# Performance work log

Hardware: AMD Instinct MI355X
Metric: run time of the kernel (lower is better)

Reference implementation:

```python
import jax, jax.numpy as jnp
import numpy as np


@jax.custom_vjp
def binarize_ste(x):
    return jnp.sign(x)


def _binarize_fwd(x):
    return jnp.sign(x), None


def _binarize_bwd(_, g):
    # straight-through estimator: pass gradient through, clamped to [-1, 1]
    return (jnp.clip(g, -1.0, 1.0),)


binarize_ste.defvjp(_binarize_fwd, _binarize_bwd)


def setup_inputs() -> dict:
    key = jax.random.key(0)
    kx, kw = jax.random.split(key)
    x = jax.random.normal(kx, (32, 128, 64, 64), dtype=jnp.float32)  # NCHW
    weight = jax.random.normal(kw, (256, 128, 3, 3), dtype=jnp.float32)  # OIHW
    return {"x": x, "weight": weight}


def reference(x, weight):
    w_bin = binarize_ste(weight)  # +/-1 (0 where weight==0, matching torch.sign)
    out = jax.lax.conv_general_dilated(
        x, w_bin,
        window_strides=(1, 1),
        padding=((1, 1), (1, 1)),
        dimension_numbers=("NCHW", "OIHW", "NCHW"),
    )
    return out
```

## Files before the change

### kernel.cpp

```cpp
#include <hip/hip_runtime.h>
#include <hip/hip_bf16.h>


typedef short bf16x8 __attribute__((ext_vector_type(8)));
typedef float f32x4 __attribute__((ext_vector_type(4)));

#define XT_ELEMS (32 * 66 * 66 * 128)
#define XT_BYTES (XT_ELEMS * 2)

__device__ __forceinline__ void glds16(const void* g, const void* l) {
    __builtin_amdgcn_global_load_lds(
        (const __attribute__((address_space(1))) void*)g,
        (__attribute__((address_space(3))) void*)l, 16, 0, 0);
}

__global__ void prep_w_kernel(const float* __restrict__ w,
                              __hip_bfloat16* __restrict__ wm) {
    int tid = blockIdx.x * 256 + threadIdx.x;
    int o = tid / 1152;
    int r = tid - o * 1152;
    int j = r >> 7;
    int c = r & 127;
    float v = w[o * 1152 + c * 9 + j];
    float s = (v > 0.f) ? 1.f : ((v < 0.f) ? -1.f : 0.f);
    wm[tid] = __float2bfloat16(s);
}

__global__ void transpose_x_kernel(const float* __restrict__ x,
                                   __hip_bfloat16* __restrict__ xt) {
    __shared__ short tl[64 * 130];
    const int t = threadIdx.x;
    const int n = blockIdx.x >> 6;
    const int h = blockIdx.x & 63;
    const float* xp = x + (size_t)n * 524288 + h * 64;
    for (int i = t; i < 8192; i += 256) {
        int w = i & 63, c = i >> 6;
        tl[w * 130 + c] = (short)__bfloat16_as_ushort(__float2bfloat16(xp[c * 4096 + w]));
    }
    uint* xtn = (uint*)(xt + (size_t)n * 66 * 66 * 128);
    {
        int row = h + 1;
        if (t < 64)       xtn[(row * 66 + 0) * 64 + t] = 0u;
        else if (t < 128) xtn[(row * 66 + 65) * 64 + (t - 64)] = 0u;
    }
    if (h == 0)  for (int i = t; i < 66 * 64; i += 256) xtn[i] = 0u;
    if (h == 63) for (int i = t; i < 66 * 64; i += 256) xtn[65 * 66 * 64 + i] = 0u;
    __syncthreads();
    uint* xo = (uint*)(xt + ((size_t)(n * 66 + h + 1) * 66 + 1) * 128);
    for (int i = t; i < 4096; i += 256) {
        int c2 = i & 63;
        int w = i >> 6;
        xo[w * 64 + c2] = *(const uint*)(tl + w * 130 + c2 * 2);
    }
}

__global__ __launch_bounds__(256, 2) void gemm_kernel(
    const __hip_bfloat16* __restrict__ xt,
    const __hip_bfloat16* __restrict__ wm,
    float* __restrict__ out) {
    __shared__ short As[128 * 64];
    __shared__ short Bw[2112 * 8];

    const int t = threadIdx.x;
    const int lane = t & 63;
    const int wv = t >> 6;
    const int px_blk = blockIdx.x;
    const int o_blk = blockIdx.y;
    const int n = px_blk >> 4;
    const int h0 = (px_blk & 15) * 4;

    const int wo = (wv & 1) * 64;
    const int wp = (wv >> 1) * 128;
    const int wpr = wp >> 6;
    const int l15 = lane & 15;
    const int quad = lane >> 4;
    const int srow = lane >> 3;
    const int sseg = lane & 7;

    const short* wmS = (const short*)wm + (o_blk * 128) * 1152;
    const short* xtS = (const short*)xt;

    f32x4 acc[4][8] = {};

    for (int cc = 0; cc < 128; cc += 64) {
        for (int kh = 0; kh < 3; ++kh) {
            const short* xw = xtS + ((size_t)(n * 66 + h0 + kh) * 66) * 128;
#pragma unroll
            for (int i = 0; i < 9; ++i) {
                int bidx = i * 4 + wv;
                if (bidx < 33) {
                    int l = bidx * 64 + lane;
                    int cell = l >> 3;
                    int q = l & 7;
                    int s = q ^ (cell & 7);
                    glds16(xw + cell * 128 + cc + s * 8, Bw + bidx * 512);
                }
            }
            for (int kw = 0; kw < 3; ++kw) {
                const int j = kh * 3 + kw;
#pragma unroll
                for (int i = 0; i < 4; ++i) {
                    int r0 = wv * 32 + i * 8;
                    int r = r0 + srow;
                    int segl = sseg ^ (r & 7);
                    glds16(wmS + r * 1152 + j * 128 + cc + segl * 8,
                           As + r0 * 64);
                }
                __syncthreads();
#pragma unroll
                for (int kf = 0; kf < 2; ++kf) {
                    bf16x8 a[4], b[8];
#pragma unroll
                    for (int i = 0; i < 4; ++i) {
                        int o = wo + i * 16 + l15;
                        int seg = (kf * 4 + quad) ^ (o & 7);
                        a[i] = *(const bf16x8*)(As + o * 64 + seg * 8);
                    }
#pragma unroll
                    for (int i = 0; i < 8; ++i) {
                        int cell = (wpr + (i >> 2)) * 66 + (i & 3) * 16 + l15 + kw;
                        int seg = (kf * 4 + quad) ^ (cell & 7);
                        b[i] = *(const bf16x8*)(Bw + cell * 64 + seg * 8);
                    }
#pragma unroll
                    for (int i = 0; i < 4; ++i)
#pragma unroll
                        for (int jj = 0; jj < 8; ++jj)
                            acc[i][jj] = __builtin_amdgcn_mfma_f32_16x16x32_bf16(
                                a[i], b[jj], acc[i][jj], 0, 0, 0);
                }
                __syncthreads();
            }
        }
    }

    const int Pbase = px_blk * 256 + wp;
#pragma unroll
    for (int i = 0; i < 4; ++i) {
#pragma unroll
        for (int jj = 0; jj < 8; ++jj) {
            const int P = Pbase + jj * 16 + l15;
            const int hw = P & 4095;
            float* op = out + (size_t)n * 1048576 + hw;
#pragma unroll
            for (int r = 0; r < 4; ++r) {
                const int o = o_blk * 128 + wo + i * 16 + quad * 4 + r;
                op[(size_t)o * 4096] = acc[i][jj][r];
            }
        }
    }
}

extern "C" void kernel_launch(void* const* d_in, const int* in_sizes, int n_in,
                              void* d_out, int out_size, void* d_ws, size_t ws_size,
                              hipStream_t stream) {
    const float* x = (const float*)d_in[0];
    const float* w = (const float*)d_in[1];
    float* out = (float*)d_out;
    __hip_bfloat16* xt = (__hip_bfloat16*)d_ws;
    __hip_bfloat16* wm = (__hip_bfloat16*)((char*)d_ws + XT_BYTES);

    prep_w_kernel<<<1152, 256, 0, stream>>>(w, wm);
    transpose_x_kernel<<<2048, 256, 0, stream>>>(x, xt);
    gemm_kernel<<<dim3(512, 2), 256, 0, stream>>>(xt, wm, out);
}
```

Measured before the change: 249.0 us.

## Double-buffer LDS staging, widen blocks to all 256 outputs, swizzle block order

The GEMM kernel now uses 512-thread blocks that cover all 256 output channels, so each input tile is loaded once instead of once per output-channel half. Weight and input tiles are double-buffered in LDS with 32-channel K-steps, and the next stage is prefetched while MFMAs run on the current one. This leaves one barrier per step where there were two. Block indices are permuted to spread neighbouring pixel tiles across the grid. The cost is larger LDS use (about 100KB per block), which may limit occupancy to one block per CU despite the launch bounds of 2.

```diff
diff --git a/kernel.cpp b/kernel.cpp
--- a/kernel.cpp
+++ b/kernel.cpp
@@ -54,87 +54,102 @@
     }
 }
 
-__global__ __launch_bounds__(256, 2) void gemm_kernel(
+__global__ __launch_bounds__(512, 2) void gemm_kernel(
     const __hip_bfloat16* __restrict__ xt,
     const __hip_bfloat16* __restrict__ wm,
     float* __restrict__ out) {
-    __shared__ short As[128 * 64];
-    __shared__ short Bw[2112 * 8];
+    __shared__ short As[2][256 * 32];
+    __shared__ short Bw[2][264 * 64];
 
     const int t = threadIdx.x;
     const int lane = t & 63;
     const int wv = t >> 6;
-    const int px_blk = blockIdx.x;
-    const int o_blk = blockIdx.y;
-    const int n = px_blk >> 4;
-    const int h0 = (px_blk & 15) * 4;
-
-    const int wo = (wv & 1) * 64;
-    const int wp = (wv >> 1) * 128;
-    const int wpr = wp >> 6;
     const int l15 = lane & 15;
     const int quad = lane >> 4;
-    const int srow = lane >> 3;
-    const int sseg = lane & 7;
 
-    const short* wmS = (const short*)wm + (o_blk * 128) * 1152;
-    const short* xtS = (const short*)xt;
+    const int bid = blockIdx.x;
+    const int px_blk = (bid & 7) * 64 + (bid >> 3);
+    const int n = px_blk >> 4;
+    const int h0 = (px_blk & 15) << 2;
+
+    const int wo = (wv >> 1) * 64;
+    const int wpr = (wv & 1) * 2;
+
+    const short* wmS = (const short*)wm;
+    const short* xtS = (const short*)xt + (size_t)(n * 66 + h0) * 66 * 128;
 
     f32x4 acc[4][8] = {};
 
-    for (int cc = 0; cc < 128; cc += 64) {
-        for (int kh = 0; kh < 3; ++kh) {
-            const short* xw = xtS + ((size_t)(n * 66 + h0 + kh) * 66) * 128;
+    auto stageA = [&](int buf, int cc, int j) {
+        const short* src = wmS + j * 128 + cc;
 #pragma unroll
-            for (int i = 0; i < 9; ++i) {
-                int bidx = i * 4 + wv;
-                if (bidx < 33) {
-                    int l = bidx * 64 + lane;
-                    int cell = l >> 3;
-                    int q = l & 7;
-                    int s = q ^ (cell & 7);
-                    glds16(xw + cell * 128 + cc + s * 8, Bw + bidx * 512);
-                }
-            }
-            for (int kw = 0; kw < 3; ++kw) {
-                const int j = kh * 3 + kw;
+        for (int i = 0; i < 2; ++i) {
+            int g = i * 8 + wv;
+            int l = g * 64 + lane;
+            int o = l >> 2, q = l & 3;
+            glds16(src + o * 1152 + ((q ^ (o & 3)) * 8), &As[buf][g * 512]);
+        }
+    };
+    auto stageB = [&](int buf, int cc, int kh) {
+        const short* src = xtS + kh * (66 * 128) + cc;
 #pragma unroll
-                for (int i = 0; i < 4; ++i) {
-                    int r0 = wv * 32 + i * 8;
-                    int r = r0 + srow;
-                    int segl = sseg ^ (r & 7);
-                    glds16(wmS + r * 1152 + j * 128 + cc + segl * 8,
-                           As + r0 * 64);
-                }
-                __syncthreads();
-#pragma unroll
-                for (int kf = 0; kf < 2; ++kf) {
-                    bf16x8 a[4], b[8];
-#pragma unroll
-                    for (int i = 0; i < 4; ++i) {
-                        int o = wo + i * 16 + l15;
-                        int seg = (kf * 4 + quad) ^ (o & 7);
-                        a[i] = *(const bf16x8*)(As + o * 64 + seg * 8);
-                    }
-#pragma unroll
-                    for (int i = 0; i < 8; ++i) {
-                        int cell = (wpr + (i >> 2)) * 66 + (i & 3) * 16 + l15 + kw;
-                        int seg = (kf * 4 + quad) ^ (cell & 7);
-                        b[i] = *(const bf16x8*)(Bw + cell * 64 + seg * 8);
-                    }
-#pragma unroll
-                    for (int i = 0; i < 4; ++i)
-#pragma unroll
-                        for (int jj = 0; jj < 8; ++jj)
-                            acc[i][jj] = __builtin_amdgcn_mfma_f32_16x16x32_bf16(
-                                a[i], b[jj], acc[i][jj], 0, 0, 0);
-                }
-                __syncthreads();
+        for (int i = 0; i < 5; ++i) {
+            int g = i * 8 + wv;
+            if (g < 33) {
+                int l = g * 64 + lane;
+                int cell = l >> 3, q = l & 7;
+                glds16(src + cell * 128 + ((q ^ (cell & 7)) * 8), &Bw[buf][g * 512]);
             }
         }
+    };
+
+    stageB(0, 0, 0);
+    stageA(0, 0, 0);
+    __syncthreads();
+
+    int Ab = 0, Bb = 0;
+    for (int s = 0; s < 36; ++s) {
+        const int s1 = s + 1;
+        if (s1 < 36) {
+            const int cc64_1 = (s1 >= 18) ? 64 : 0;
+            const int r1 = s1 % 18;
+            const int kh1 = r1 / 6;
+            const int sub1 = (r1 % 6) / 3;
+            const int kw1 = r1 % 3;
+            if (s1 % 6 == 0) stageB(Bb ^ 1, cc64_1, kh1);
+            stageA(Ab ^ 1, cc64_1 + sub1 * 32, kh1 * 3 + kw1);
+        }
+        {
+            const int r = s % 18;
+            const int sub = (r % 6) / 3;
+            const int kw = r % 3;
+            const short* A_ = As[Ab];
+            const short* B_ = Bw[Bb];
+            bf16x8 a[4], b[8];
+#pragma unroll
+            for (int i = 0; i < 4; ++i) {
+                int o = wo + i * 16 + l15;
+                a[i] = *(const bf16x8*)(A_ + o * 32 + ((quad ^ (o & 3)) * 8));
+            }
+#pragma unroll
+            for (int i = 0; i < 8; ++i) {
+                int cell = (wpr + (i >> 2)) * 66 + (i & 3) * 16 + l15 + kw;
+                int seg = (sub * 4 + quad) ^ (cell & 7);
+                b[i] = *(const bf16x8*)(B_ + cell * 64 + seg * 8);
+            }
+#pragma unroll
+            for (int i = 0; i < 4; ++i)
+#pragma unroll
+                for (int jj = 0; jj < 8; ++jj)
+                    acc[i][jj] = __builtin_amdgcn_mfma_f32_16x16x32_bf16(
+                        a[i], b[jj], acc[i][jj], 0, 0, 0);
+        }
+        __syncthreads();
+        Ab ^= 1;
+        if (s1 % 6 == 0) Bb ^= 1;
     }
 
-    const int Pbase = px_blk * 256 + wp;
+    const int Pbase = px_blk * 256 + (wv & 1) * 128;
 #pragma unroll
     for (int i = 0; i < 4; ++i) {
 #pragma unroll
@@ -144,7 +159,7 @@
             float* op = out + (size_t)n * 1048576 + hw;
 #pragma unroll
             for (int r = 0; r < 4; ++r) {
-                const int o = o_blk * 128 + wo + i * 16 + quad * 4 + r;
+                const int o = wo + i * 16 + quad * 4 + r;
                 op[(size_t)o * 4096] = acc[i][jj][r];
             }
         }
@@ -162,5 +177,5 @@
 
     prep_w_kernel<<<1152, 256, 0, stream>>>(w, wm);
     transpose_x_kernel<<<2048, 256, 0, stream>>>(x, xt);
-    gemm_kernel<<<dim3(512, 2), 256, 0, stream>>>(xt, wm, out);
+    gemm_kernel<<<512, 512, 0, stream>>>(xt, wm, out);
 }
```

Result: slower. 271.9 us (+9.2%).

## Double-buffer input tile in LDS and load weights directly into registers

Applied to the files above, without the earlier changes.

The input-row tile now uses two LDS buffers, so the next (channel-chunk, kh) stage is prefetched with async global-to-LDS loads while the current stage runs its MFMAs. The weight tile no longer goes through LDS; each wave reads its bf16x8 A fragments straight from global memory (L2-resident) into registers. This removes the per-kw barriers and the weight staging. Block indices are also remapped to interleave pixel blocks across batch images. The trade-off is extra global-load latency on the weight reads and higher register pressure.

```diff
diff --git a/kernel.cpp b/kernel.cpp
--- a/kernel.cpp
+++ b/kernel.cpp
@@ -58,13 +58,16 @@
     const __hip_bfloat16* __restrict__ xt,
     const __hip_bfloat16* __restrict__ wm,
     float* __restrict__ out) {
-    __shared__ short As[128 * 64];
-    __shared__ short Bw[2112 * 8];
+    __shared__ short Bw[2][264 * 64];
 
     const int t = threadIdx.x;
     const int lane = t & 63;
     const int wv = t >> 6;
-    const int px_blk = blockIdx.x;
+    const int l15 = lane & 15;
+    const int quad = lane >> 4;
+
+    const int bid = blockIdx.x;
+    const int px_blk = (bid & 7) * 64 + (bid >> 3);
     const int o_blk = blockIdx.y;
     const int n = px_blk >> 4;
     const int h0 = (px_blk & 15) * 4;
@@ -72,66 +75,68 @@
     const int wo = (wv & 1) * 64;
     const int wp = (wv >> 1) * 128;
     const int wpr = wp >> 6;
-    const int l15 = lane & 15;
-    const int quad = lane >> 4;
-    const int srow = lane >> 3;
-    const int sseg = lane & 7;
 
-    const short* wmS = (const short*)wm + (o_blk * 128) * 1152;
     const short* xtS = (const short*)xt;
+    const short* aBase = (const short*)wm +
+        (size_t)(o_blk * 128 + wo + l15) * 1152 + quad * 8;
 
     f32x4 acc[4][8] = {};
 
-    for (int cc = 0; cc < 128; cc += 64) {
-        for (int kh = 0; kh < 3; ++kh) {
-            const short* xw = xtS + ((size_t)(n * 66 + h0 + kh) * 66) * 128;
+    auto stageB = [&](int buf, int cc, int kh) {
+        const short* src = xtS + ((size_t)(n * 66 + h0 + kh) * 66) * 128 + cc;
 #pragma unroll
-            for (int i = 0; i < 9; ++i) {
-                int bidx = i * 4 + wv;
-                if (bidx < 33) {
-                    int l = bidx * 64 + lane;
-                    int cell = l >> 3;
-                    int q = l & 7;
-                    int s = q ^ (cell & 7);
-                    glds16(xw + cell * 128 + cc + s * 8, Bw + bidx * 512);
-                }
-            }
-            for (int kw = 0; kw < 3; ++kw) {
-                const int j = kh * 3 + kw;
-#pragma unroll
-                for (int i = 0; i < 4; ++i) {
-                    int r0 = wv * 32 + i * 8;
-                    int r = r0 + srow;
-                    int segl = sseg ^ (r & 7);
-                    glds16(wmS + r * 1152 + j * 128 + cc + segl * 8,
-                           As + r0 * 64);
-                }
-                __syncthreads();
-#pragma unroll
-                for (int kf = 0; kf < 2; ++kf) {
-                    bf16x8 a[4], b[8];
-#pragma unroll
-                    for (int i = 0; i < 4; ++i) {
-                        int o = wo + i * 16 + l15;
-                        int seg = (kf * 4 + quad) ^ (o & 7);
-                        a[i] = *(const bf16x8*)(As + o * 64 + seg * 8);
-                    }
-#pragma unroll
-                    for (int i = 0; i < 8; ++i) {
-                        int cell = (wpr + (i >> 2)) * 66 + (i & 3) * 16 + l15 + kw;
-                        int seg = (kf * 4 + quad) ^ (cell & 7);
-                        b[i] = *(const bf16x8*)(Bw + cell * 64 + seg * 8);
-                    }
-#pragma unroll
-                    for (int i = 0; i < 4; ++i)
-#pragma unroll
-                        for (int jj = 0; jj < 8; ++jj)
-                            acc[i][jj] = __builtin_amdgcn_mfma_f32_16x16x32_bf16(
-                                a[i], b[jj], acc[i][jj], 0, 0, 0);
-                }
-                __syncthreads();
+        for (int i = 0; i < 9; ++i) {
+            int g = i * 4 + wv;
+            if (g < 33) {
+                int l = g * 64 + lane;
+                int cell = l >> 3, q = l & 7;
+                glds16(src + cell * 128 + ((q ^ (cell & 7)) * 8),
+                       &Bw[buf][g * 512]);
             }
         }
+    };
+
+    stageB(0, 0, 0);
+    __syncthreads();
+
+    int buf = 0;
+    for (int s = 0; s < 6; ++s) {
+        const int cc = (s >= 3) ? 64 : 0;
+        const int kh = (s >= 3) ? (s - 3) : s;
+        if (s + 1 < 6) {
+            const int s1 = s + 1;
+            stageB(buf ^ 1, (s1 >= 3) ? 64 : 0, (s1 >= 3) ? (s1 - 3) : s1);
+        }
+#pragma unroll
+        for (int kw = 0; kw < 3; ++kw) {
+            const int j = kh * 3 + kw;
+            const short* ap = aBase + j * 128 + cc;
+            bf16x8 a0[4], a1[4];
+#pragma unroll
+            for (int i = 0; i < 4; ++i)
+                a0[i] = *(const bf16x8*)(ap + (size_t)i * 16 * 1152);
+#pragma unroll
+            for (int i = 0; i < 4; ++i)
+                a1[i] = *(const bf16x8*)(ap + (size_t)i * 16 * 1152 + 32);
+#pragma unroll
+            for (int kf = 0; kf < 2; ++kf) {
+                bf16x8 b[8];
+#pragma unroll
+                for (int i = 0; i < 8; ++i) {
+                    int cell = (wpr + (i >> 2)) * 66 + (i & 3) * 16 + l15 + kw;
+                    int seg = (kf * 4 + quad) ^ (cell & 7);
+                    b[i] = *(const bf16x8*)(&Bw[buf][cell * 64 + seg * 8]);
+                }
+#pragma unroll
+                for (int i = 0; i < 4; ++i)
+#pragma unroll
+                    for (int jj = 0; jj < 8; ++jj)
+                        acc[i][jj] = __builtin_amdgcn_mfma_f32_16x16x32_bf16(
+                            kf ? a1[i] : a0[i], b[jj], acc[i][jj], 0, 0, 0);
+            }
+        }
+        __syncthreads();
+        buf ^= 1;
     }
 
     const int Pbase = px_blk * 256 + wp;
```

Measured after the change: 408.5 us. 1.64x slower.

## Software-pipeline conv GEMM with double-buffered weight tiles and manual waitcnts

Applied to the files above, without the earlier changes.

Restructures the implicit-GEMM main loop into a flat 18-step pipeline. Weight tiles are double-buffered in LDS and prefetched two steps ahead, and the next input row is staged right after the second-half fragment reads, with explicit vmcnt/lgkmcnt waits and raw barriers replacing __syncthreads. This is meant to hide global-to-LDS load latency behind MFMA work. It also remaps block indices for locality and raises wave priority around the MFMA bursts. The hand-counted waitcnts are fragile: a miscount could race on the LDS buffers.

```diff
diff --git a/kernel.cpp b/kernel.cpp
--- a/kernel.cpp
+++ b/kernel.cpp
@@ -7,6 +7,10 @@
 
 #define XT_ELEMS (32 * 66 * 66 * 128)
 #define XT_BYTES (XT_ELEMS * 2)
+
+#define VMW4 asm volatile("s_waitcnt vmcnt(4)" ::: "memory")
+#define VMW0 asm volatile("s_waitcnt vmcnt(0)" ::: "memory")
+#define LGKM0 asm volatile("s_waitcnt lgkmcnt(0)" ::: "memory")
 
 __device__ __forceinline__ void glds16(const void* g, const void* l) {
     __builtin_amdgcn_global_load_lds(
@@ -58,79 +62,122 @@
     const __hip_bfloat16* __restrict__ xt,
     const __hip_bfloat16* __restrict__ wm,
     float* __restrict__ out) {
-    __shared__ short As[128 * 64];
-    __shared__ short Bw[2112 * 8];
+    __shared__ short As[2][128 * 64];
+    __shared__ short Bw[264 * 64];
 
     const int t = threadIdx.x;
     const int lane = t & 63;
     const int wv = t >> 6;
-    const int px_blk = blockIdx.x;
-    const int o_blk = blockIdx.y;
-    const int n = px_blk >> 4;
-    const int h0 = (px_blk & 15) * 4;
-
-    const int wo = (wv & 1) * 64;
-    const int wp = (wv >> 1) * 128;
-    const int wpr = wp >> 6;
     const int l15 = lane & 15;
     const int quad = lane >> 4;
     const int srow = lane >> 3;
     const int sseg = lane & 7;
 
+    const int bid = blockIdx.x;
+    const int px_blk = (bid & 7) * 64 + (bid >> 3);
+    const int o_blk = blockIdx.y;
+    const int n = px_blk >> 4;
+    const int h0 = (px_blk & 15) * 4;
+
+    const int wo = (wv & 1) * 64;
+    const int wp = (wv >> 1) * 128;
+    const int wpr = wp >> 6;
+
     const short* wmS = (const short*)wm + (o_blk * 128) * 1152;
-    const short* xtS = (const short*)xt;
+    const short* xtB = (const short*)xt + ((size_t)(n * 66 + h0) * 66) * 128;
 
     f32x4 acc[4][8] = {};
 
-    for (int cc = 0; cc < 128; cc += 64) {
-        for (int kh = 0; kh < 3; ++kh) {
-            const short* xw = xtS + ((size_t)(n * 66 + h0 + kh) * 66) * 128;
-#pragma unroll
-            for (int i = 0; i < 9; ++i) {
-                int bidx = i * 4 + wv;
-                if (bidx < 33) {
-                    int l = bidx * 64 + lane;
-                    int cell = l >> 3;
-                    int q = l & 7;
-                    int s = q ^ (cell & 7);
-                    glds16(xw + cell * 128 + cc + s * 8, Bw + bidx * 512);
-                }
+    auto stageA = [&](int buf, int cc, int j) {
+#pragma unroll
+        for (int i = 0; i < 4; ++i) {
+            int r0 = wv * 32 + i * 8;
+            int r = r0 + srow;
+            int segl = sseg ^ (r & 7);
+            glds16(wmS + r * 1152 + j * 128 + cc + segl * 8,
+                   &As[buf][r0 * 64]);
+        }
+    };
+    auto stageB = [&](int cc, int kh) {
+        const short* src = xtB + kh * (66 * 128) + cc;
+#pragma unroll
+        for (int i = 0; i < 9; ++i) {
+            int bidx = i * 4 + wv;
+            if (bidx > 32) bidx = 32;
+            int l = bidx * 64 + lane;
+            int cell = l >> 3;
+            int q = l & 7;
+            glds16(src + cell * 128 + ((q ^ (cell & 7)) * 8),
+                   &Bw[bidx * 512]);
+        }
+    };
+
+    stageB(0, 0);
+    stageA(0, 0, 0);
+    stageA(1, 0, 1);
+
+    int ab = 0;
+    for (int s = 0; s < 6; ++s) {
+        const int cc = (s >= 3) ? 64 : 0;
+        const int kh = s % 3;
+#pragma unroll
+        for (int kw = 0; kw < 3; ++kw) {
+            const int p = s * 3 + kw;
+            if (p == 17) { VMW0; } else { VMW4; }
+            __builtin_amdgcn_s_barrier();
+            {
+                bf16x8 a[4], b[8];
+#pragma unroll
+                for (int i = 0; i < 4; ++i) {
+                    int o = wo + i * 16 + l15;
+                    a[i] = *(const bf16x8*)(&As[ab][o * 64 + ((quad ^ (o & 7)) * 8)]);
+                }
+#pragma unroll
+                for (int i = 0; i < 8; ++i) {
+                    int cell = (wpr + (i >> 2)) * 66 + (i & 3) * 16 + l15 + kw;
+                    int seg = quad ^ (cell & 7);
+                    b[i] = *(const bf16x8*)(&Bw[cell * 64 + seg * 8]);
+                }
+                __builtin_amdgcn_s_setprio(1);
+#pragma unroll
+                for (int i = 0; i < 4; ++i)
+#pragma unroll
+                    for (int jj = 0; jj < 8; ++jj)
+                        acc[i][jj] = __builtin_amdgcn_mfma_f32_16x16x32_bf16(
+                            a[i], b[jj], acc[i][jj], 0, 0, 0);
+                __builtin_amdgcn_s_setprio(0);
             }
-            for (int kw = 0; kw < 3; ++kw) {
-                const int j = kh * 3 + kw;
+            {
+                bf16x8 a[4], b[8];
 #pragma unroll
                 for (int i = 0; i < 4; ++i) {
-                    int r0 = wv * 32 + i * 8;
-                    int r = r0 + srow;
-                    int segl = sseg ^ (r & 7);
-                    glds16(wmS + r * 1152 + j * 128 + cc + segl * 8,
-                           As + r0 * 64);
-                }
-                __syncthreads();
-#pragma unroll
-                for (int kf = 0; kf < 2; ++kf) {
-                    bf16x8 a[4], b[8];
-#pragma unroll
-                    for (int i = 0; i < 4; ++i) {
-                        int o = wo + i * 16 + l15;
-                        int seg = (kf * 4 + quad) ^ (o & 7);
-                        a[i] = *(const bf16x8*)(As + o * 64 + seg * 8);
-                    }
-#pragma unroll
-                    for (int i = 0; i < 8; ++i) {
-                        int cell = (wpr + (i >> 2)) * 66 + (i & 3) * 16 + l15 + kw;
-                        int seg = (kf * 4 + quad) ^ (cell & 7);
-                        b[i] = *(const bf16x8*)(Bw + cell * 64 + seg * 8);
-                    }
-#pragma unroll
-                    for (int i = 0; i < 4; ++i)
-#pragma unroll
-                        for (int jj = 0; jj < 8; ++jj)
-                            acc[i][jj] = __builtin_amdgcn_mfma_f32_16x16x32_bf16(
-                                a[i], b[jj], acc[i][jj], 0, 0, 0);
-                }
-                __syncthreads();
+                    int o = wo + i * 16 + l15;
+                    a[i] = *(const bf16x8*)(&As[ab][o * 64 + (((4 + quad) ^ (o & 7)) * 8)]);
+                }
+#pragma unroll
+                for (int i = 0; i < 8; ++i) {
+                    int cell = (wpr + (i >> 2)) * 66 + (i & 3) * 16 + l15 + kw;
+                    int seg = (4 + quad) ^ (cell & 7);
+                    b[i] = *(const bf16x8*)(&Bw[cell * 64 + seg * 8]);
+                }
+                LGKM0;
+                __builtin_amdgcn_s_barrier();
+                if (kw == 2 && s < 5)
+                    stageB((s + 1) >= 3 ? 64 : 0, (s + 1) % 3);
+                if (p <= 15) {
+                    int pn = p + 2, sn = pn / 3, kwn = pn % 3;
+                    stageA(ab, (sn >= 3) ? 64 : 0, (sn % 3) * 3 + kwn);
+                }
+                __builtin_amdgcn_s_setprio(1);
+#pragma unroll
+                for (int i = 0; i < 4; ++i)
+#pragma unroll
+                    for (int jj = 0; jj < 8; ++jj)
+                        acc[i][jj] = __builtin_amdgcn_mfma_f32_16x16x32_bf16(
+                            a[i], b[jj], acc[i][jj], 0, 0, 0);
+                __builtin_amdgcn_s_setprio(0);
             }
+            ab ^= 1;
         }
     }
 
```

Result: slower. 399.7 us (+60.6%).
